# Kernel tuning notes

Measured on AMD Instinct MI355X. Metric: run time of the kernel, lower is better.

Reference implementation:

```python
import jax, jax.numpy as jnp
import numpy as np

B, S, D, H = 4, 2048, 1024, 16
HEAD = D // H
DENOM = float(np.sqrt(D))  # NOTE: original divides by sqrt(hidden_size), not sqrt(head_size)


def setup_inputs() -> dict:
    key = jax.random.key(0)
    ks = jax.random.split(key, 5)
    scale = 1.0 / np.sqrt(D)
    return {
        "hidden_state": jax.random.normal(ks[0], (B, S, D), dtype=jnp.float32),
        "attention_mask": jnp.ones((B, S), dtype=jnp.int32),  # unused in forward (faithful to source)
        "w_q": jax.random.normal(ks[1], (D, D), dtype=jnp.float32) * scale,
        "w_k": jax.random.normal(ks[2], (D, D), dtype=jnp.float32) * scale,
        "w_v": jax.random.normal(ks[3], (D, D), dtype=jnp.float32) * scale,
        "w_o": jax.random.normal(ks[4], (D, D), dtype=jnp.float32) * scale,
    }


def _split_heads(x):
    # [B, S, D] -> [B, H, S, head]
    b, s, _ = x.shape
    return x.reshape(b, s, H, HEAD).transpose(0, 2, 1, 3)


def reference(hidden_state, attention_mask, w_q, w_k, w_v, w_o):
    # nn.Linear(bias=False): y = x @ W^T with W of shape [out, in]
    q = _split_heads(hidden_state @ w_q.T)  # [B, H, S, head]
    k = _split_heads(hidden_state @ w_k.T)
    v = _split_heads(hidden_state @ w_v.T)
    qk = jnp.einsum("bhqd,bhkd->bhqk", q, k) / DENOM  # scale = 1/sqrt(hidden_size)
    attn = jax.nn.softmax(qk, axis=-1)  # attention_mask is NOT applied (matches source)
    ctx = jnp.einsum("bhqk,bhkd->bhqd", attn, v)  # [B, H, S, head]
    ctx = ctx.transpose(0, 2, 1, 3).reshape(hidden_state.shape[0], hidden_state.shape[1], D)
    return ctx @ w_o.T
```

## Files before the change

### kernel.cpp

```cpp
#include <hip/hip_runtime.h>
#include <hip/hip_bf16.h>
#include <math.h>

typedef __bf16 bf16x8 __attribute__((ext_vector_type(8)));
typedef __bf16 bf16x2 __attribute__((ext_vector_type(2)));
typedef float f32x4 __attribute__((ext_vector_type(4)));
typedef float f32x16 __attribute__((ext_vector_type(16)));
typedef unsigned u32x2v __attribute__((ext_vector_type(2)));
typedef unsigned u32x4v __attribute__((ext_vector_type(4)));
typedef unsigned short u16;

#define QSCALE 0.04508422002778011f

__device__ __forceinline__ u16 f2b(float f) {
  union { float f; unsigned u; } x; x.f = f;
  unsigned r = x.u + 0x7fffu + ((x.u >> 16) & 1u);
  return (u16)(r >> 16);
}

__device__ __forceinline__ unsigned pkbf(float a, float b) {
  bf16x2 t = { (__bf16)a, (__bf16)b };
  return __builtin_bit_cast(unsigned, t);
}

#define GLOAD_LDS16(g, s)                                                      \
  __builtin_amdgcn_global_load_lds(                                            \
      (__attribute__((address_space(1))) void*)(void*)(g),                     \
      (__attribute__((address_space(3))) void*)(s), 16, 0, 0)

__global__ void cast_bf16_kernel(const float* __restrict__ in, u16* __restrict__ out,
                                 int n4) {
  int i = blockIdx.x * blockDim.x + threadIdx.x;
  int stride = gridDim.x * blockDim.x;
  for (; i < n4; i += stride) {
    float4 v = ((const float4*)in)[i];
    ushort4 o;
    o.x = f2b(v.x); o.y = f2b(v.y); o.z = f2b(v.z); o.w = f2b(v.w);
    ((ushort4*)out)[i] = o;
  }
}

__global__ void cast_w4_kernel(const float* __restrict__ wq, const float* __restrict__ wk,
                               const float* __restrict__ wv, const float* __restrict__ wo,
                               u16* __restrict__ wqkv, u16* __restrict__ wob) {
  const int w = blockIdx.y;
  const float* src = (w == 0) ? wq : (w == 1) ? wk : (w == 2) ? wv : wo;
  u16* dst = (w < 3) ? wqkv + (size_t)w * 1024 * 1024 : wob;
  const float scale = (w == 0) ? QSCALE : 1.0f;
  const int n4 = 1024 * 1024 / 4;
  int i = blockIdx.x * blockDim.x + threadIdx.x;
  int stride = gridDim.x * blockDim.x;
  for (; i < n4; i += stride) {
    float4 v = ((const float4*)src)[i];
    ushort4 o;
    o.x = f2b(v.x * scale); o.y = f2b(v.y * scale);
    o.z = f2b(v.z * scale); o.w = f2b(v.w * scale);
    ((ushort4*)dst)[i] = o;
  }
}

__global__ __launch_bounds__(256) void gemm_qkv(const u16* __restrict__ A,
                                                const u16* __restrict__ Bw,
                                                u16* __restrict__ Qo,
                                                u16* __restrict__ Ko,
                                                u16* __restrict__ Vt) {
  __shared__ u16 As[128 * 32];
  __shared__ u16 Bs[128 * 32];
  const int tid = threadIdx.x;
  const int wid = tid >> 6, lane = tid & 63;
  const int fr = lane & 15, fg = lane >> 4;
  const int wr = wid >> 1, wc = wid & 1;
  const int m0 = blockIdx.y * 128, n0 = blockIdx.x * 128;
  const int K = 1024;

  f32x4 acc[4][4] = {};

  for (int kt = 0; kt < K; kt += 32) {
#pragma unroll
    for (int i2 = 0; i2 < 2; ++i2) {
      int c = i2 * 256 + tid;
      int row = c >> 2, kc = c & 3;
      GLOAD_LDS16(A + (size_t)(m0 + row) * K + kt + kc * 8, (char*)As + c * 16);
      GLOAD_LDS16(Bw + (size_t)(n0 + row) * K + kt + kc * 8, (char*)Bs + c * 16);
    }
    __syncthreads();

    bf16x8 af[4], bfr[4];
#pragma unroll
    for (int m = 0; m < 4; ++m)
      af[m] = *(const bf16x8*)((const char*)As + (wr * 64 + m * 16 + fr) * 64 + fg * 16);
#pragma unroll
    for (int n = 0; n < 4; ++n)
      bfr[n] = *(const bf16x8*)((const char*)Bs + (wc * 64 + n * 16 + fr) * 64 + fg * 16);
#pragma unroll
    for (int m = 0; m < 4; ++m)
#pragma unroll
      for (int n = 0; n < 4; ++n)
        acc[m][n] = __builtin_amdgcn_mfma_f32_16x16x32_bf16(af[m], bfr[n], acc[m][n], 0, 0, 0);
    __syncthreads();
  }

  const int region = n0 >> 10;
#pragma unroll
  for (int m = 0; m < 4; ++m)
#pragma unroll
    for (int n = 0; n < 4; ++n) {
      int gr = m0 + wr * 64 + m * 16 + fg * 4;
      int gc = n0 + wc * 64 + n * 16 + fr;
      if (region == 2) {
        int vc = gc - 2048;
        int hh = vc >> 6, d = vc & 63, bb = gr >> 11, s0 = gr & 2047;
        ushort4 o;
        o.x = f2b(acc[m][n][0]); o.y = f2b(acc[m][n][1]);
        o.z = f2b(acc[m][n][2]); o.w = f2b(acc[m][n][3]);
        *(ushort4*)(Vt + (((size_t)bb * 16 + hh) * 64 + d) * 2048 + s0) = o;
      } else {
        u16* dst = (region == 0) ? Qo : Ko;
        int cc = gc & 1023;
#pragma unroll
        for (int j = 0; j < 4; ++j)
          dst[(size_t)(gr + j) * 1024 + cc] = f2b(acc[m][n][j]);
      }
    }
}

__global__ __launch_bounds__(256) void gemm_o(const u16* __restrict__ A,
                                              const u16* __restrict__ B,
                                              float* __restrict__ Cout) {
  __shared__ u16 As[128 * 32];
  __shared__ u16 Bs[128 * 32];
  const int tid = threadIdx.x;
  const int wid = tid >> 6, lane = tid & 63;
  const int fr = lane & 15, fg = lane >> 4;
  const int wr = wid >> 1, wc = wid & 1;
  const int m0 = blockIdx.y * 128, n0 = blockIdx.x * 128;
  const int K = 1024, N = 1024;

  f32x4 acc[4][4] = {};

  for (int kt = 0; kt < K; kt += 32) {
#pragma unroll
    for (int i2 = 0; i2 < 2; ++i2) {
      int c = i2 * 256 + tid;
      int row = c >> 2, kc = c & 3;
      GLOAD_LDS16(A + (size_t)(m0 + row) * K + kt + kc * 8, (char*)As + c * 16);
      GLOAD_LDS16(B + (size_t)(n0 + row) * K + kt + kc * 8, (char*)Bs + c * 16);
    }
    __syncthreads();

    bf16x8 af[4], bfr[4];
#pragma unroll
    for (int m = 0; m < 4; ++m)
      af[m] = *(const bf16x8*)((const char*)As + (wr * 64 + m * 16 + fr) * 64 + fg * 16);
#pragma unroll
    for (int n = 0; n < 4; ++n)
      bfr[n] = *(const bf16x8*)((const char*)Bs + (wc * 64 + n * 16 + fr) * 64 + fg * 16);
#pragma unroll
    for (int m = 0; m < 4; ++m)
#pragma unroll
      for (int n = 0; n < 4; ++n)
        acc[m][n] = __builtin_amdgcn_mfma_f32_16x16x32_bf16(af[m], bfr[n], acc[m][n], 0, 0, 0);
    __syncthreads();
  }

#pragma unroll
  for (int m = 0; m < 4; ++m)
#pragma unroll
    for (int n = 0; n < 4; ++n) {
      int gr = m0 + wr * 64 + m * 16 + fg * 4;
      int gc = n0 + wc * 64 + n * 16 + fr;
#pragma unroll
      for (int j = 0; j < 4; ++j)
        Cout[(size_t)(gr + j) * N + gc] = acc[m][n][j];
    }
}

__global__ __launch_bounds__(256, 4) void attn_fwd(const u16* __restrict__ Q,
                                                   const u16* __restrict__ Kg,
                                                   const u16* __restrict__ Vtg,
                                                   u16* __restrict__ O) {
  __shared__ u16 Ks[2][64 * 64];
  __shared__ u16 Vs[2][64 * 64];
  const int tid = threadIdx.x;
  const int wid = tid >> 6, lane = tid & 63;
  const int lq = lane & 31, hi = lane >> 5;
  const int id = blockIdx.x;
  const int swz = (id & 7) * 128 + (id >> 3);
  const int qb = swz & 15, bh = swz >> 4;
  const int b = bh >> 4, h = bh & 15;
  const size_t tokBase = (size_t)b * 2048 * 1024 + h * 64;
  const size_t vBase = (size_t)bh * 64 * 2048;
  const int q0 = qb * 128 + wid * 32;

  bf16x8 qf[4];
#pragma unroll
  for (int s = 0; s < 4; ++s)
    qf[s] = *(const bf16x8*)(Q + tokBase + (size_t)(q0 + lq) * 1024 + s * 16 + hi * 8);

  const bf16x8 ones8 = { (__bf16)1.f, (__bf16)1.f, (__bf16)1.f, (__bf16)1.f,
                         (__bf16)1.f, (__bf16)1.f, (__bf16)1.f, (__bf16)1.f };

  f32x16 acc0 = {}, acc1 = {}, accl = {};

  const int skey = tid >> 3, sdc = tid & 7;
  const int sdg = sdc ^ (skey & 7);
  const int skey2 = (tid + 256) >> 3, sdc2 = tid & 7;
  const int sdg2 = sdc2 ^ (skey2 & 7);

#define STAGE(bb_, k0_) do {                                                          \
    GLOAD_LDS16(Kg + tokBase + (size_t)((k0_) + skey) * 1024 + sdg * 8,               \
                (char*)Ks[bb_] + tid * 16);                                           \
    GLOAD_LDS16(Kg + tokBase + (size_t)((k0_) + skey2) * 1024 + sdg2 * 8,             \
                (char*)Ks[bb_] + (tid + 256) * 16);                                   \
    GLOAD_LDS16(Vtg + vBase + (size_t)skey * 2048 + (k0_) + sdg * 8,                  \
                (char*)Vs[bb_] + tid * 16);                                           \
    GLOAD_LDS16(Vtg + vBase + (size_t)skey2 * 2048 + (k0_) + sdg2 * 8,                \
                (char*)Vs[bb_] + (tid + 256) * 16);                                   \
  } while (0)

  STAGE(0, 0);
  for (int t = 0; t < 32; ++t) {
    const int bb = t & 1;
    __syncthreads();
    if (t < 31) STAGE(bb ^ 1, (t + 1) * 64);

    f32x16 sv0 = {}, sv1 = {};
    __builtin_amdgcn_s_setprio(1);
#pragma unroll
    for (int s = 0; s < 4; ++s) {
      bf16x8 kf0 = *(const bf16x8*)((const char*)Ks[bb] + lq * 128 +
                                    ((s * 32 + hi * 16) ^ ((lq & 7) << 4)));
      sv0 = __builtin_amdgcn_mfma_f32_32x32x16_bf16(kf0, qf[s], sv0, 0, 0, 0);
      bf16x8 kf1 = *(const bf16x8*)((const char*)Ks[bb] + (32 + lq) * 128 +
                                    ((s * 32 + hi * 16) ^ ((lq & 7) << 4)));
      sv1 = __builtin_amdgcn_mfma_f32_32x32x16_bf16(kf1, qf[s], sv1, 0, 0, 0);
    }
    __builtin_amdgcn_s_setprio(0);

#pragma unroll
    for (int i = 0; i < 16; ++i) sv0[i] = __builtin_amdgcn_exp2f(sv0[i]);
#pragma unroll
    for (int i = 0; i < 16; ++i) sv1[i] = __builtin_amdgcn_exp2f(sv1[i]);

    bf16x8 pa[4];
#pragma unroll
    for (int kb = 0; kb < 2; ++kb) {
#pragma unroll
      for (int hh = 0; hh < 2; ++hh) {
        const f32x16& pv = kb ? sv1 : sv0;
        const int rb = hh * 8;
        unsigned w01 = pkbf(pv[rb + 0], pv[rb + 1]);
        unsigned w23 = pkbf(pv[rb + 2], pv[rb + 3]);
        unsigned w45 = pkbf(pv[rb + 4], pv[rb + 5]);
        unsigned w67 = pkbf(pv[rb + 6], pv[rb + 7]);
        u32x2v ra = __builtin_amdgcn_permlane32_swap(w01, w45, false, false);
        u32x2v rc = __builtin_amdgcn_permlane32_swap(w23, w67, false, false);
        u32x4v fw = { ra[0], rc[0], ra[1], rc[1] };
        pa[kb * 2 + hh] = __builtin_bit_cast(bf16x8, fw);
      }
    }

    __builtin_amdgcn_s_setprio(1);
#pragma unroll
    for (int s = 0; s < 4; ++s) {
      bf16x8 bv0 = *(const bf16x8*)((const char*)Vs[bb] + lq * 128 +
                                    ((s * 32 + hi * 16) ^ ((lq & 7) << 4)));
      acc0 = __builtin_amdgcn_mfma_f32_32x32x16_bf16(pa[s], bv0, acc0, 0, 0, 0);
      bf16x8 bv1 = *(const bf16x8*)((const char*)Vs[bb] + (32 + lq) * 128 +
                                    ((s * 32 + hi * 16) ^ ((lq & 7) << 4)));
      acc1 = __builtin_amdgcn_mfma_f32_32x32x16_bf16(pa[s], bv1, acc1, 0, 0, 0);
      accl = __builtin_amdgcn_mfma_f32_32x32x16_bf16(pa[s], ones8, accl, 0, 0, 0);
    }
    __builtin_amdgcn_s_setprio(0);
  }
#undef STAGE

#pragma unroll
  for (int r = 0; r < 16; ++r) {
    const int q = (r & 3) + 8 * (r >> 2) + 4 * hi;
    const float iv = 1.0f / accl[r];
    const size_t row = (size_t)(b * 2048 + q0 + q) * 1024 + h * 64;
    O[row + lq]      = f2b(acc0[r] * iv);
    O[row + 32 + lq] = f2b(acc1[r] * iv);
  }
}

extern "C" void kernel_launch(void* const* d_in, const int* in_sizes, int n_in,
                              void* d_out, int out_size, void* d_ws, size_t ws_size,
                              hipStream_t stream) {
  const float* hs = (const float*)d_in[0];
  const float* wq = (const float*)d_in[2];
  const float* wk = (const float*)d_in[3];
  const float* wv = (const float*)d_in[4];
  const float* wo = (const float*)d_in[5];

  const size_t TOK = 8192, DD = 1024;
  u16* hsb  = (u16*)d_ws;
  u16* wqkv = hsb + TOK * DD;
  u16* wob  = wqkv + 3 * DD * DD;
  u16* Qb   = wob + DD * DD;
  u16* Kb   = Qb + TOK * DD;
  u16* Vtg  = Kb + TOK * DD;
  u16* Cb   = Vtg + TOK * DD;

  cast_bf16_kernel<<<2048, 256, 0, stream>>>(hs, hsb, (int)(TOK * DD / 4));
  cast_w4_kernel<<<dim3(128, 4), 256, 0, stream>>>(wq, wk, wv, wo, wqkv, wob);

  gemm_qkv<<<dim3(24, 64), 256, 0, stream>>>(hsb, wqkv, Qb, Kb, Vtg);

  attn_fwd<<<dim3(1024), 256, 0, stream>>>(Qb, Kb, Vtg, Cb);

  gemm_o<<<dim3(8, 64), 256, 0, stream>>>(Cb, wob, (float*)d_out);
}
```

Baseline: 214.1 us.

## Process two query tiles per wave in attention and compute row sums from exponentials

Each wave now handles 64 query rows as two 32-row tiles, so every K and V fragment read from LDS feeds twice as many MFMAs. The block covers 256 queries and the grid is halved. The softmax denominator is no longer an extra MFMA against a ones vector; it is built by summing the exponentiated scores in registers and reducing across lanes with shuffles. In exchange, register pressure roughly doubles, so launch bounds drop from 4 to 2 blocks per CU, which lowers occupancy and latency hiding.

New measurement: 199.6 us. 6.8% less time.

```diff
diff --git a/kernel.cpp b/kernel.cpp
--- a/kernel.cpp
+++ b/kernel.cpp
@@ -175,7 +175,7 @@
     }
 }
 
-__global__ __launch_bounds__(256, 4) void attn_fwd(const u16* __restrict__ Q,
+__global__ __launch_bounds__(256, 2) void attn_fwd(const u16* __restrict__ Q,
                                                    const u16* __restrict__ Kg,
                                                    const u16* __restrict__ Vtg,
                                                    u16* __restrict__ O) {
@@ -185,27 +185,27 @@
   const int wid = tid >> 6, lane = tid & 63;
   const int lq = lane & 31, hi = lane >> 5;
   const int id = blockIdx.x;
-  const int swz = (id & 7) * 128 + (id >> 3);
-  const int qb = swz & 15, bh = swz >> 4;
+  const int swz = (id & 7) * 64 + (id >> 3);
+  const int qb = swz & 7, bh = swz >> 3;
   const int b = bh >> 4, h = bh & 15;
   const size_t tokBase = (size_t)b * 2048 * 1024 + h * 64;
   const size_t vBase = (size_t)bh * 64 * 2048;
-  const int q0 = qb * 128 + wid * 32;
-
-  bf16x8 qf[4];
-#pragma unroll
-  for (int s = 0; s < 4; ++s)
-    qf[s] = *(const bf16x8*)(Q + tokBase + (size_t)(q0 + lq) * 1024 + s * 16 + hi * 8);
-
-  const bf16x8 ones8 = { (__bf16)1.f, (__bf16)1.f, (__bf16)1.f, (__bf16)1.f,
-                         (__bf16)1.f, (__bf16)1.f, (__bf16)1.f, (__bf16)1.f };
-
-  f32x16 acc0 = {}, acc1 = {}, accl = {};
+  const int q0 = qb * 256 + wid * 64;
+
+  bf16x8 qfA[4], qfB[4];
+#pragma unroll
+  for (int s = 0; s < 4; ++s) {
+    qfA[s] = *(const bf16x8*)(Q + tokBase + (size_t)(q0 + lq) * 1024 + s * 16 + hi * 8);
+    qfB[s] = *(const bf16x8*)(Q + tokBase + (size_t)(q0 + 32 + lq) * 1024 + s * 16 + hi * 8);
+  }
+
+  f32x16 accA0 = {}, accA1 = {}, accB0 = {}, accB1 = {};
+  f32x16 lsvA = {}, lsvB = {};
 
   const int skey = tid >> 3, sdc = tid & 7;
   const int sdg = sdc ^ (skey & 7);
-  const int skey2 = (tid + 256) >> 3, sdc2 = tid & 7;
-  const int sdg2 = sdc2 ^ (skey2 & 7);
+  const int skey2 = (tid + 256) >> 3;
+  const int sdg2 = sdc ^ (skey2 & 7);
 
 #define STAGE(bb_, k0_) do {                                                          \
     GLOAD_LDS16(Kg + tokBase + (size_t)((k0_) + skey) * 1024 + sdg * 8,               \
@@ -224,39 +224,60 @@
     __syncthreads();
     if (t < 31) STAGE(bb ^ 1, (t + 1) * 64);
 
-    f32x16 sv0 = {}, sv1 = {};
+    f32x16 svA0 = {}, svA1 = {}, svB0 = {}, svB1 = {};
     __builtin_amdgcn_s_setprio(1);
 #pragma unroll
     for (int s = 0; s < 4; ++s) {
       bf16x8 kf0 = *(const bf16x8*)((const char*)Ks[bb] + lq * 128 +
                                     ((s * 32 + hi * 16) ^ ((lq & 7) << 4)));
-      sv0 = __builtin_amdgcn_mfma_f32_32x32x16_bf16(kf0, qf[s], sv0, 0, 0, 0);
       bf16x8 kf1 = *(const bf16x8*)((const char*)Ks[bb] + (32 + lq) * 128 +
                                     ((s * 32 + hi * 16) ^ ((lq & 7) << 4)));
-      sv1 = __builtin_amdgcn_mfma_f32_32x32x16_bf16(kf1, qf[s], sv1, 0, 0, 0);
+      svA0 = __builtin_amdgcn_mfma_f32_32x32x16_bf16(kf0, qfA[s], svA0, 0, 0, 0);
+      svB0 = __builtin_amdgcn_mfma_f32_32x32x16_bf16(kf0, qfB[s], svB0, 0, 0, 0);
+      svA1 = __builtin_amdgcn_mfma_f32_32x32x16_bf16(kf1, qfA[s], svA1, 0, 0, 0);
+      svB1 = __builtin_amdgcn_mfma_f32_32x32x16_bf16(kf1, qfB[s], svB1, 0, 0, 0);
     }
     __builtin_amdgcn_s_setprio(0);
 
 #pragma unroll
-    for (int i = 0; i < 16; ++i) sv0[i] = __builtin_amdgcn_exp2f(sv0[i]);
-#pragma unroll
-    for (int i = 0; i < 16; ++i) sv1[i] = __builtin_amdgcn_exp2f(sv1[i]);
-
-    bf16x8 pa[4];
+    for (int i = 0; i < 16; ++i) svA0[i] = __builtin_amdgcn_exp2f(svA0[i]);
+#pragma unroll
+    for (int i = 0; i < 16; ++i) svA1[i] = __builtin_amdgcn_exp2f(svA1[i]);
+#pragma unroll
+    for (int i = 0; i < 16; ++i) svB0[i] = __builtin_amdgcn_exp2f(svB0[i]);
+#pragma unroll
+    for (int i = 0; i < 16; ++i) svB1[i] = __builtin_amdgcn_exp2f(svB1[i]);
+    lsvA += svA0; lsvA += svA1;
+    lsvB += svB0; lsvB += svB1;
+
+    bf16x8 paA[4], paB[4];
 #pragma unroll
     for (int kb = 0; kb < 2; ++kb) {
 #pragma unroll
       for (int hh = 0; hh < 2; ++hh) {
-        const f32x16& pv = kb ? sv1 : sv0;
         const int rb = hh * 8;
-        unsigned w01 = pkbf(pv[rb + 0], pv[rb + 1]);
-        unsigned w23 = pkbf(pv[rb + 2], pv[rb + 3]);
-        unsigned w45 = pkbf(pv[rb + 4], pv[rb + 5]);
-        unsigned w67 = pkbf(pv[rb + 6], pv[rb + 7]);
-        u32x2v ra = __builtin_amdgcn_permlane32_swap(w01, w45, false, false);
-        u32x2v rc = __builtin_amdgcn_permlane32_swap(w23, w67, false, false);
-        u32x4v fw = { ra[0], rc[0], ra[1], rc[1] };
-        pa[kb * 2 + hh] = __builtin_bit_cast(bf16x8, fw);
+        {
+          const f32x16& pv = kb ? svA1 : svA0;
+          unsigned w01 = pkbf(pv[rb + 0], pv[rb + 1]);
+          unsigned w23 = pkbf(pv[rb + 2], pv[rb + 3]);
+          unsigned w45 = pkbf(pv[rb + 4], pv[rb + 5]);
+          unsigned w67 = pkbf(pv[rb + 6], pv[rb + 7]);
+          u32x2v ra = __builtin_amdgcn_permlane32_swap(w01, w45, false, false);
+          u32x2v rc = __builtin_amdgcn_permlane32_swap(w23, w67, false, false);
+          u32x4v fw = { ra[0], rc[0], ra[1], rc[1] };
+          paA[kb * 2 + hh] = __builtin_bit_cast(bf16x8, fw);
+        }
+        {
+          const f32x16& pv = kb ? svB1 : svB0;
+          unsigned w01 = pkbf(pv[rb + 0], pv[rb + 1]);
+          unsigned w23 = pkbf(pv[rb + 2], pv[rb + 3]);
+          unsigned w45 = pkbf(pv[rb + 4], pv[rb + 5]);
+          unsigned w67 = pkbf(pv[rb + 6], pv[rb + 7]);
+          u32x2v ra = __builtin_amdgcn_permlane32_swap(w01, w45, false, false);
+          u32x2v rc = __builtin_amdgcn_permlane32_swap(w23, w67, false, false);
+          u32x4v fw = { ra[0], rc[0], ra[1], rc[1] };
+          paB[kb * 2 + hh] = __builtin_bit_cast(bf16x8, fw);
+        }
       }
     }
 
@@ -265,23 +286,34 @@
     for (int s = 0; s < 4; ++s) {
       bf16x8 bv0 = *(const bf16x8*)((const char*)Vs[bb] + lq * 128 +
                                     ((s * 32 + hi * 16) ^ ((lq & 7) << 4)));
-      acc0 = __builtin_amdgcn_mfma_f32_32x32x16_bf16(pa[s], bv0, acc0, 0, 0, 0);
       bf16x8 bv1 = *(const bf16x8*)((const char*)Vs[bb] + (32 + lq) * 128 +
                                     ((s * 32 + hi * 16) ^ ((lq & 7) << 4)));
-      acc1 = __builtin_amdgcn_mfma_f32_32x32x16_bf16(pa[s], bv1, acc1, 0, 0, 0);
-      accl = __builtin_amdgcn_mfma_f32_32x32x16_bf16(pa[s], ones8, accl, 0, 0, 0);
+      accA0 = __builtin_amdgcn_mfma_f32_32x32x16_bf16(paA[s], bv0, accA0, 0, 0, 0);
+      accA1 = __builtin_amdgcn_mfma_f32_32x32x16_bf16(paA[s], bv1, accA1, 0, 0, 0);
+      accB0 = __builtin_amdgcn_mfma_f32_32x32x16_bf16(paB[s], bv0, accB0, 0, 0, 0);
+      accB1 = __builtin_amdgcn_mfma_f32_32x32x16_bf16(paB[s], bv1, accB1, 0, 0, 0);
     }
     __builtin_amdgcn_s_setprio(0);
   }
 #undef STAGE
 
+  float totA = 0.f, totB = 0.f;
+#pragma unroll
+  for (int i = 0; i < 16; ++i) { totA += lsvA[i]; totB += lsvB[i]; }
+  totA += __shfl_xor(totA, 32);
+  totB += __shfl_xor(totB, 32);
+  const float invA = 1.0f / totA, invB = 1.0f / totB;
 #pragma unroll
   for (int r = 0; r < 16; ++r) {
     const int q = (r & 3) + 8 * (r >> 2) + 4 * hi;
-    const float iv = 1.0f / accl[r];
-    const size_t row = (size_t)(b * 2048 + q0 + q) * 1024 + h * 64;
-    O[row + lq]      = f2b(acc0[r] * iv);
-    O[row + 32 + lq] = f2b(acc1[r] * iv);
+    const float ivA = __shfl(invA, q);
+    const float ivB = __shfl(invB, q);
+    const size_t rowA = (size_t)(b * 2048 + q0 + q) * 1024 + h * 64;
+    const size_t rowB = (size_t)(b * 2048 + q0 + 32 + q) * 1024 + h * 64;
+    O[rowA + lq]      = f2b(accA0[r] * ivA);
+    O[rowA + 32 + lq] = f2b(accA1[r] * ivA);
+    O[rowB + lq]      = f2b(accB0[r] * ivB);
+    O[rowB + 32 + lq] = f2b(accB1[r] * ivB);
   }
 }
 
@@ -308,7 +340,7 @@
 
   gemm_qkv<<<dim3(24, 64), 256, 0, stream>>>(hsb, wqkv, Qb, Kb, Vtg);
 
-  attn_fwd<<<dim3(1024), 256, 0, stream>>>(Qb, Kb, Vtg, Cb);
+  attn_fwd<<<dim3(512), 256, 0, stream>>>(Qb, Kb, Vtg, Cb);
 
   gemm_o<<<dim3(8, 64), 256, 0, stream>>>(Cb, wob, (float*)d_out);
 }
```

## Double query rows per warp and triple-buffer K/V tiles in attention

Applied to the files above, without the earlier changes.

Each warp now handles 64 query rows (two 32-row sets) instead of 32, so every K/V fragment read from LDS feeds twice as many MFMAs and the grid halves to 512 blocks. The K/V staging moves from a double buffer to a three-slot ring with explicit vmcnt waits and raw barriers, so loads run two tiles ahead of compute. The trade is more registers (launch bounds drop from 4 to 2 blocks per SM), lower occupancy and a larger LDS footprint. The gemm_o store also hardcodes N as 1024.

New measurement: 201.1 us. 6.1% less time.

```diff
diff --git a/kernel.cpp b/kernel.cpp
--- a/kernel.cpp
+++ b/kernel.cpp
@@ -27,6 +27,12 @@
   __builtin_amdgcn_global_load_lds(                                            \
       (__attribute__((address_space(1))) void*)(void*)(g),                     \
       (__attribute__((address_space(3))) void*)(s), 16, 0, 0)
+
+#define VMCNT8 asm volatile("s_waitcnt vmcnt(8)" ::: "memory")
+#define VMCNT4 asm volatile("s_waitcnt vmcnt(4)" ::: "memory")
+#define VMCNT0 asm volatile("s_waitcnt vmcnt(0)" ::: "memory")
+#define WAITL  asm volatile("s_waitcnt lgkmcnt(0)" ::: "memory")
+#define SBAR   __builtin_amdgcn_s_barrier()
 
 __global__ void cast_bf16_kernel(const float* __restrict__ in, u16* __restrict__ out,
                                  int n4) {
@@ -171,117 +177,157 @@
       int gc = n0 + wc * 64 + n * 16 + fr;
 #pragma unroll
       for (int j = 0; j < 4; ++j)
-        Cout[(size_t)(gr + j) * N + gc] = acc[m][n][j];
+        Cout[(size_t)(gr + j) * 1024 + gc] = acc[m][n][j];
     }
 }
 
-__global__ __launch_bounds__(256, 4) void attn_fwd(const u16* __restrict__ Q,
+__global__ __launch_bounds__(256, 2) void attn_fwd(const u16* __restrict__ Q,
                                                    const u16* __restrict__ Kg,
                                                    const u16* __restrict__ Vtg,
                                                    u16* __restrict__ O) {
-  __shared__ u16 Ks[2][64 * 64];
-  __shared__ u16 Vs[2][64 * 64];
+  __shared__ u16 Ks[3 * 64 * 64];
+  __shared__ u16 Vs[3 * 64 * 64];
   const int tid = threadIdx.x;
   const int wid = tid >> 6, lane = tid & 63;
   const int lq = lane & 31, hi = lane >> 5;
   const int id = blockIdx.x;
-  const int swz = (id & 7) * 128 + (id >> 3);
-  const int qb = swz & 15, bh = swz >> 4;
+  const int swz = (id & 7) * 64 + (id >> 3);
+  const int qb = swz & 7, bh = swz >> 3;
   const int b = bh >> 4, h = bh & 15;
   const size_t tokBase = (size_t)b * 2048 * 1024 + h * 64;
   const size_t vBase = (size_t)bh * 64 * 2048;
-  const int q0 = qb * 128 + wid * 32;
-
-  bf16x8 qf[4];
-#pragma unroll
-  for (int s = 0; s < 4; ++s)
-    qf[s] = *(const bf16x8*)(Q + tokBase + (size_t)(q0 + lq) * 1024 + s * 16 + hi * 8);
+  const int q0 = qb * 256 + wid * 64;
+
+  bf16x8 qfA[4], qfB[4];
+#pragma unroll
+  for (int s = 0; s < 4; ++s) {
+    qfA[s] = *(const bf16x8*)(Q + tokBase + (size_t)(q0 + lq) * 1024 + s * 16 + hi * 8);
+    qfB[s] = *(const bf16x8*)(Q + tokBase + (size_t)(q0 + 32 + lq) * 1024 + s * 16 + hi * 8);
+  }
 
   const bf16x8 ones8 = { (__bf16)1.f, (__bf16)1.f, (__bf16)1.f, (__bf16)1.f,
                          (__bf16)1.f, (__bf16)1.f, (__bf16)1.f, (__bf16)1.f };
 
-  f32x16 acc0 = {}, acc1 = {}, accl = {};
+  f32x16 accA0 = {}, accA1 = {}, accB0 = {}, accB1 = {};
+  f32x16 acclA = {}, acclB = {};
 
   const int skey = tid >> 3, sdc = tid & 7;
   const int sdg = sdc ^ (skey & 7);
-  const int skey2 = (tid + 256) >> 3, sdc2 = tid & 7;
-  const int sdg2 = sdc2 ^ (skey2 & 7);
-
-#define STAGE(bb_, k0_) do {                                                          \
+  const int skey2 = (tid + 256) >> 3;
+  const int sdg2 = sdc ^ (skey2 & 7);
+
+#define STAGE(off_, k0_) do {                                                         \
     GLOAD_LDS16(Kg + tokBase + (size_t)((k0_) + skey) * 1024 + sdg * 8,               \
-                (char*)Ks[bb_] + tid * 16);                                           \
+                (char*)Ks + (off_) + tid * 16);                                       \
     GLOAD_LDS16(Kg + tokBase + (size_t)((k0_) + skey2) * 1024 + sdg2 * 8,             \
-                (char*)Ks[bb_] + (tid + 256) * 16);                                   \
+                (char*)Ks + (off_) + (tid + 256) * 16);                               \
     GLOAD_LDS16(Vtg + vBase + (size_t)skey * 2048 + (k0_) + sdg * 8,                  \
-                (char*)Vs[bb_] + tid * 16);                                           \
+                (char*)Vs + (off_) + tid * 16);                                       \
     GLOAD_LDS16(Vtg + vBase + (size_t)skey2 * 2048 + (k0_) + sdg2 * 8,                \
-                (char*)Vs[bb_] + (tid + 256) * 16);                                   \
+                (char*)Vs + (off_) + (tid + 256) * 16);                               \
   } while (0)
 
+#define TILE(bo_) do {                                                                \
+    const char* Kb_ = (const char*)Ks + (bo_);                                        \
+    const char* Vb_ = (const char*)Vs + (bo_);                                        \
+    f32x16 svA0 = {}, svA1 = {}, svB0 = {}, svB1 = {};                                \
+    __builtin_amdgcn_s_setprio(1);                                                    \
+    _Pragma("unroll") for (int s = 0; s < 4; ++s) {                                   \
+      bf16x8 kf0 = *(const bf16x8*)(Kb_ + lq * 128 +                                  \
+                                    ((s * 32 + hi * 16) ^ ((lq & 7) << 4)));          \
+      bf16x8 kf1 = *(const bf16x8*)(Kb_ + (32 + lq) * 128 +                           \
+                                    ((s * 32 + hi * 16) ^ ((lq & 7) << 4)));          \
+      svA0 = __builtin_amdgcn_mfma_f32_32x32x16_bf16(kf0, qfA[s], svA0, 0, 0, 0);     \
+      svB0 = __builtin_amdgcn_mfma_f32_32x32x16_bf16(kf0, qfB[s], svB0, 0, 0, 0);     \
+      svA1 = __builtin_amdgcn_mfma_f32_32x32x16_bf16(kf1, qfA[s], svA1, 0, 0, 0);     \
+      svB1 = __builtin_amdgcn_mfma_f32_32x32x16_bf16(kf1, qfB[s], svB1, 0, 0, 0);     \
+    }                                                                                 \
+    __builtin_amdgcn_s_setprio(0);                                                    \
+    _Pragma("unroll") for (int i = 0; i < 16; ++i)                                    \
+      svA0[i] = __builtin_amdgcn_exp2f(svA0[i]);                                      \
+    _Pragma("unroll") for (int i = 0; i < 16; ++i)                                    \
+      svA1[i] = __builtin_amdgcn_exp2f(svA1[i]);                                      \
+    _Pragma("unroll") for (int i = 0; i < 16; ++i)                                    \
+      svB0[i] = __builtin_amdgcn_exp2f(svB0[i]);                                      \
+    _Pragma("unroll") for (int i = 0; i < 16; ++i)                                    \
+      svB1[i] = __builtin_amdgcn_exp2f(svB1[i]);                                      \
+    bf16x8 paA[4], paB[4];                                                            \
+    _Pragma("unroll") for (int kb = 0; kb < 2; ++kb) {                                \
+      _Pragma("unroll") for (int hh = 0; hh < 2; ++hh) {                              \
+        const int rb = hh * 8;                                                        \
+        {                                                                             \
+          const f32x16& pv = kb ? svA1 : svA0;                                        \
+          unsigned w01 = pkbf(pv[rb + 0], pv[rb + 1]);                                \
+          unsigned w23 = pkbf(pv[rb + 2], pv[rb + 3]);                                \
+          unsigned w45 = pkbf(pv[rb + 4], pv[rb + 5]);                                \
+          unsigned w67 = pkbf(pv[rb + 6], pv[rb + 7]);                                \
+          u32x2v ra = __builtin_amdgcn_permlane32_swap(w01, w45, false, false);       \
+          u32x2v rc = __builtin_amdgcn_permlane32_swap(w23, w67, false, false);       \
+          u32x4v fw = { ra[0], rc[0], ra[1], rc[1] };                                 \
+          paA[kb * 2 + hh] = __builtin_bit_cast(bf16x8, fw);                          \
+        }                                                                             \
+        {                                                                             \
+          const f32x16& pv = kb ? svB1 : svB0;                                        \
+          unsigned w01 = pkbf(pv[rb + 0], pv[rb + 1]);                                \
+          unsigned w23 = pkbf(pv[rb + 2], pv[rb + 3]);                                \
+          unsigned w45 = pkbf(pv[rb + 4], pv[rb + 5]);                                \
+          unsigned w67 = pkbf(pv[rb + 6], pv[rb + 7]);                                \
+          u32x2v ra = __builtin_amdgcn_permlane32_swap(w01, w45, false, false);       \
+          u32x2v rc = __builtin_amdgcn_permlane32_swap(w23, w67, false, false);       \
+          u32x4v fw = { ra[0], rc[0], ra[1], rc[1] };                                 \
+          paB[kb * 2 + hh] = __builtin_bit_cast(bf16x8, fw);                          \
+        }                                                                             \
+      }                                                                               \
+    }                                                                                 \
+    __builtin_amdgcn_s_setprio(1);                                                    \
+    _Pragma("unroll") for (int s = 0; s < 4; ++s) {                                   \
+      bf16x8 bv0 = *(const bf16x8*)(Vb_ + lq * 128 +                                  \
+                                    ((s * 32 + hi * 16) ^ ((lq & 7) << 4)));          \
+      bf16x8 bv1 = *(const bf16x8*)(Vb_ + (32 + lq) * 128 +                           \
+                                    ((s * 32 + hi * 16) ^ ((lq & 7) << 4)));          \
+      accA0 = __builtin_amdgcn_mfma_f32_32x32x16_bf16(paA[s], bv0, accA0, 0, 0, 0);   \
+      accA1 = __builtin_amdgcn_mfma_f32_32x32x16_bf16(paA[s], bv1, accA1, 0, 0, 0);   \
+      accB0 = __builtin_amdgcn_mfma_f32_32x32x16_bf16(paB[s], bv0, accB0, 0, 0, 0);   \
+      accB1 = __builtin_amdgcn_mfma_f32_32x32x16_bf16(paB[s], bv1, accB1, 0, 0, 0);   \
+      acclA = __builtin_amdgcn_mfma_f32_32x32x16_bf16(paA[s], ones8, acclA, 0, 0, 0); \
+      acclB = __builtin_amdgcn_mfma_f32_32x32x16_bf16(paB[s], ones8, acclB, 0, 0, 0); \
+    }                                                                                 \
+    __builtin_amdgcn_s_setprio(0);                                                    \
+  } while (0)
+
   STAGE(0, 0);
-  for (int t = 0; t < 32; ++t) {
-    const int bb = t & 1;
-    __syncthreads();
-    if (t < 31) STAGE(bb ^ 1, (t + 1) * 64);
-
-    f32x16 sv0 = {}, sv1 = {};
-    __builtin_amdgcn_s_setprio(1);
-#pragma unroll
-    for (int s = 0; s < 4; ++s) {
-      bf16x8 kf0 = *(const bf16x8*)((const char*)Ks[bb] + lq * 128 +
-                                    ((s * 32 + hi * 16) ^ ((lq & 7) << 4)));
-      sv0 = __builtin_amdgcn_mfma_f32_32x32x16_bf16(kf0, qf[s], sv0, 0, 0, 0);
-      bf16x8 kf1 = *(const bf16x8*)((const char*)Ks[bb] + (32 + lq) * 128 +
-                                    ((s * 32 + hi * 16) ^ ((lq & 7) << 4)));
-      sv1 = __builtin_amdgcn_mfma_f32_32x32x16_bf16(kf1, qf[s], sv1, 0, 0, 0);
-    }
-    __builtin_amdgcn_s_setprio(0);
-
-#pragma unroll
-    for (int i = 0; i < 16; ++i) sv0[i] = __builtin_amdgcn_exp2f(sv0[i]);
-#pragma unroll
-    for (int i = 0; i < 16; ++i) sv1[i] = __builtin_amdgcn_exp2f(sv1[i]);
-
-    bf16x8 pa[4];
-#pragma unroll
-    for (int kb = 0; kb < 2; ++kb) {
-#pragma unroll
-      for (int hh = 0; hh < 2; ++hh) {
-        const f32x16& pv = kb ? sv1 : sv0;
-        const int rb = hh * 8;
-        unsigned w01 = pkbf(pv[rb + 0], pv[rb + 1]);
-        unsigned w23 = pkbf(pv[rb + 2], pv[rb + 3]);
-        unsigned w45 = pkbf(pv[rb + 4], pv[rb + 5]);
-        unsigned w67 = pkbf(pv[rb + 6], pv[rb + 7]);
-        u32x2v ra = __builtin_amdgcn_permlane32_swap(w01, w45, false, false);
-        u32x2v rc = __builtin_amdgcn_permlane32_swap(w23, w67, false, false);
-        u32x4v fw = { ra[0], rc[0], ra[1], rc[1] };
-        pa[kb * 2 + hh] = __builtin_bit_cast(bf16x8, fw);
-      }
-    }
-
-    __builtin_amdgcn_s_setprio(1);
-#pragma unroll
-    for (int s = 0; s < 4; ++s) {
-      bf16x8 bv0 = *(const bf16x8*)((const char*)Vs[bb] + lq * 128 +
-                                    ((s * 32 + hi * 16) ^ ((lq & 7) << 4)));
-      acc0 = __builtin_amdgcn_mfma_f32_32x32x16_bf16(pa[s], bv0, acc0, 0, 0, 0);
-      bf16x8 bv1 = *(const bf16x8*)((const char*)Vs[bb] + (32 + lq) * 128 +
-                                    ((s * 32 + hi * 16) ^ ((lq & 7) << 4)));
-      acc1 = __builtin_amdgcn_mfma_f32_32x32x16_bf16(pa[s], bv1, acc1, 0, 0, 0);
-      accl = __builtin_amdgcn_mfma_f32_32x32x16_bf16(pa[s], ones8, accl, 0, 0, 0);
-    }
-    __builtin_amdgcn_s_setprio(0);
-  }
+  STAGE(8192, 64);
+
+  int bo = 0, so = 16384;
+  for (int t = 0; t < 30; ++t) {
+    STAGE(so, (t + 2) * 64);
+    VMCNT8;
+    SBAR;
+    TILE(bo);
+    WAITL;
+    SBAR;
+    bo += 8192; if (bo == 24576) bo = 0;
+    so += 8192; if (so == 24576) so = 0;
+  }
+  VMCNT4; SBAR;
+  TILE(0);
+  WAITL; SBAR;
+  VMCNT0; SBAR;
+  TILE(8192);
+#undef TILE
 #undef STAGE
 
 #pragma unroll
   for (int r = 0; r < 16; ++r) {
     const int q = (r & 3) + 8 * (r >> 2) + 4 * hi;
-    const float iv = 1.0f / accl[r];
-    const size_t row = (size_t)(b * 2048 + q0 + q) * 1024 + h * 64;
-    O[row + lq]      = f2b(acc0[r] * iv);
-    O[row + 32 + lq] = f2b(acc1[r] * iv);
+    const float ivA = 1.0f / acclA[r];
+    const float ivB = 1.0f / acclB[r];
+    const size_t rowA = (size_t)(b * 2048 + q0 + q) * 1024 + h * 64;
+    const size_t rowB = (size_t)(b * 2048 + q0 + 32 + q) * 1024 + h * 64;
+    O[rowA + lq]      = f2b(accA0[r] * ivA);
+    O[rowA + 32 + lq] = f2b(accA1[r] * ivA);
+    O[rowB + lq]      = f2b(accB0[r] * ivB);
+    O[rowB + 32 + lq] = f2b(accB1[r] * ivB);
   }
 }
 
@@ -308,7 +354,7 @@
 
   gemm_qkv<<<dim3(24, 64), 256, 0, stream>>>(hsb, wqkv, Qb, Kb, Vtg);
 
-  attn_fwd<<<dim3(1024), 256, 0, stream>>>(Qb, Kb, Vtg, Cb);
+  attn_fwd<<<dim3(512), 256, 0, stream>>>(Qb, Kb, Vtg, Cb);
 
   gemm_o<<<dim3(8, 64), 256, 0, stream>>>(Cb, wob, (float*)d_out);
 }
```
